# Optimization experiments

Measured on AMD Instinct MI355X. Metric: run time of the kernel, lower is better.

The kernel has to match this reference:

```python
import jax, jax.numpy as jnp
import numpy as np

LATENT, COND, NEURONS, NHID = 64, 96, 128, 3
EPS = 1e-5


def setup_inputs() -> dict:
    key = jax.random.key(0)
    ks = jax.random.split(key, 20)
    B, N = 1024, 512
    z0 = jax.random.normal(ks[0], (B, LATENT), jnp.float32)
    # monotone time grid in [0,1]
    t = jnp.cumsum(jax.random.uniform(ks[1], (B, N, 1), jnp.float32), axis=1)
    t = t / t[:, -1:, :]
    condition = jax.random.normal(ks[2], (B, N, COND), jnp.float32)
    dims = [LATENT + COND] + [NEURONS] * NHID
    inp = {"z0": z0, "t": t, "condition": condition}
    for i in range(NHID):
        din, dout = dims[i], dims[i + 1]
        inp[f"W{i}"] = jax.random.normal(ks[3 + 4 * i], (din, dout), jnp.float32) / np.sqrt(din)
        inp[f"b{i}"] = jnp.zeros((dout,), jnp.float32)
        inp[f"g{i}"] = jnp.ones((dout,), jnp.float32)
        inp[f"beta{i}"] = jnp.zeros((dout,), jnp.float32)
    inp["Wo"] = jax.random.normal(ks[16], (NEURONS, LATENT), jnp.float32) / np.sqrt(NEURONS)
    inp["bo"] = jnp.zeros((LATENT,), jnp.float32)
    return inp


def _layer_norm(x, g, b):
    mu = jnp.mean(x, axis=-1, keepdims=True)
    var = jnp.var(x, axis=-1, keepdims=True)
    return (x - mu) * jax.lax.rsqrt(var + EPS) * g + b


def reference(z0, t, condition,
              W0, b0, g0, beta0,
              W1, b1, g1, beta1,
              W2, b2, g2, beta2,
              Wo, bo):
    # dropout is inference-mode identity
    hidden = [(W0, b0, g0, beta0), (W1, b1, g1, beta1), (W2, b2, g2, beta2)]

    def mlp(x):
        h = x
        for (W, b, g, be) in hidden:
            h = jnp.tanh(_layer_norm(h @ W + b, g, be))
        return h @ Wo + bo

    # time-major sequences for scan: [N-1, B, ...]
    cond_seq = jnp.swapaxes(condition[:, :-1, :], 0, 1)
    dt_seq = jnp.swapaxes(t[:, 1:, 0] - t[:, :-1, 0], 0, 1)[..., None]

    def step(z, inp):
        cond_i, dt_i = inp
        dz = mlp(jnp.concatenate([z, cond_i], axis=-1))
        z_next = z + dt_i * dz
        return z_next, z_next

    _, zs = jax.lax.scan(step, z0, (cond_seq, dt_seq))  # [N-1, B, D]
    z_traj = jnp.concatenate([z0[None], zs], axis=0)  # [N, B, D]
    return jnp.swapaxes(z_traj, 0, 1)  # [B, N, D]
```

## Files before the change

### kernel.cpp

```cpp
#include <hip/hip_runtime.h>
#include <stdint.h>

#define NSEQ 512
#define XS 168
#define AS 136
#define PS 36
#define EPS 1e-5f

typedef short bfrag __attribute__((ext_vector_type(8)));
typedef float f4 __attribute__((ext_vector_type(4)));
#define MFMA16 __builtin_amdgcn_mfma_f32_16x16x32_bf16

__device__ __forceinline__ unsigned short f2bf(float f){
  uint32_t u = __float_as_uint(f);
  u += 0x7FFFu + ((u>>16)&1u);
  return (unsigned short)(u>>16);
}
__device__ __forceinline__ uint32_t pk2bf(float a, float b){
  uint32_t r;
  asm("v_cvt_pk_bf16_f32 %0, %1, %2" : "=v"(r) : "v"(a), "v"(b));
  return r;
}
__device__ __forceinline__ float tanh_fast(float v){
  float e = __builtin_amdgcn_exp2f(v * 2.8853900817779268f);
  float r = __builtin_amdgcn_rcpf(e + 1.f);
  return fmaf(-2.f, r, 1.f);
}
__device__ __forceinline__ void lds_barrier(){
  asm volatile("s_waitcnt lgkmcnt(0)" ::: "memory");
  __builtin_amdgcn_s_barrier();
  asm volatile("" ::: "memory");
}

__device__ __forceinline__ void stats_write(const float (&h0)[4], const float (&h1)[4],
                                            float* __restrict__ part,
                                            const int w, const int lg, const int lc){
  const float s = ((h0[0]+h0[1])+(h0[2]+h0[3])) + ((h1[0]+h1[1])+(h1[2]+h1[3]));
  const float q = (fmaf(h0[0],h0[0], h0[1]*h0[1]) + fmaf(h0[2],h0[2], h0[3]*h0[3]))
                + (fmaf(h1[0],h1[0], h1[1]*h1[1]) + fmaf(h1[2],h1[2], h1[3]*h1[3]));
  *(float2*)(part + lc*PS + (w*4+lg)*2) = make_float2(s, q);
}

__device__ __forceinline__ void ln_tanh_store(const float (&h0)[4], const float (&h1)[4],
    const float (&gd)[2][4], const float (&bed)[2][4],
    const float* __restrict__ part, unsigned short* __restrict__ actb,
    const int w, const int lg, const int lc){
  const float* pr = part + lc*PS;
  const f4 p0=*(const f4*)(pr),    p1=*(const f4*)(pr+4),  p2=*(const f4*)(pr+8),  p3=*(const f4*)(pr+12);
  const f4 p4=*(const f4*)(pr+16), p5=*(const f4*)(pr+20), p6=*(const f4*)(pr+24), p7=*(const f4*)(pr+28);
  const float ss = (((p0.x+p0.z)+(p1.x+p1.z)) + ((p2.x+p2.z)+(p3.x+p3.z)))
                 + (((p4.x+p4.z)+(p5.x+p5.z)) + ((p6.x+p6.z)+(p7.x+p7.z)));
  const float qq = (((p0.y+p0.w)+(p1.y+p1.w)) + ((p2.y+p2.w)+(p3.y+p3.w)))
                 + (((p4.y+p4.w)+(p5.y+p5.w)) + ((p6.y+p6.w)+(p7.y+p7.w)));
  const float mu = ss * 0.0078125f;
  const float rs = rsqrtf(fmaf(qq, 0.0078125f, -mu*mu) + EPS);
  float e0[4], e1[4];
#pragma unroll
  for (int g=0; g<4; ++g){
    e0[g] = tanh_fast(fmaf((h0[g]-mu)*rs, gd[0][g], bed[0][g]));
    e1[g] = tanh_fast(fmaf((h1[g]-mu)*rs, gd[1][g], bed[1][g]));
  }
  uint4 pk4;
  pk4.x = pk2bf(e0[0],e0[1]); pk4.y = pk2bf(e0[2],e0[3]);
  pk4.z = pk2bf(e1[0],e1[1]); pk4.w = pk2bf(e1[2],e1[3]);
  *(uint4*)(actb + lc*AS + w*32 + lg*8) = pk4;
}

__global__ __launch_bounds__(256, 1)
void latent_ode_v9(const float* __restrict__ z0, const float* __restrict__ tt,
                   const float* __restrict__ cond,
                   const float* __restrict__ W0, const float* __restrict__ b0,
                   const float* __restrict__ g0, const float* __restrict__ be0,
                   const float* __restrict__ W1, const float* __restrict__ b1,
                   const float* __restrict__ g1, const float* __restrict__ be1,
                   const float* __restrict__ W2, const float* __restrict__ b2,
                   const float* __restrict__ g2, const float* __restrict__ be2,
                   const float* __restrict__ Wo, const float* __restrict__ bo,
                   float* __restrict__ out)
{
  __shared__ __align__(16) unsigned short xin[16*XS];
  __shared__ __align__(16) unsigned short act[16*AS];
  __shared__ __align__(16) float part[16*PS];

  const int t  = threadIdx.x;
  const int w  = t >> 6;
  const int l  = t & 63;
  const int lg = l >> 4;
  const int lc = l & 15;
  const int r0 = blockIdx.x * 16;
  const int zcol = w*16 + lg*4;

  bfrag A0z[2][2], A0c[2][3], A1f[2][4], A2f[2][4], Aof[4];
#pragma unroll
  for (int nt=0; nt<2; ++nt){
    const int col = w*32 + nt*4 + ((lc>>2)<<3) + (lc&3);
#pragma unroll
    for (int kt=0; kt<2; ++kt){
      union { bfrag v; unsigned short u[8]; } r;
#pragma unroll
      for (int j=0; j<8; ++j) r.u[j] = f2bf(W0[(size_t)(kt*32 + lg*8 + j)*128 + col]);
      A0z[nt][kt] = r.v;
    }
#pragma unroll
    for (int s=0; s<3; ++s){
      union { bfrag v; unsigned short u[8]; } r;
#pragma unroll
      for (int j=0; j<8; ++j) r.u[j] = f2bf(W0[(size_t)(64 + s*32 + lg*8 + j)*128 + col]);
      A0c[nt][s] = r.v;
    }
#pragma unroll
    for (int kt=0; kt<4; ++kt){
      union { bfrag v; unsigned short u[8]; } r1, r2;
#pragma unroll
      for (int j=0; j<8; ++j){
        const int k = kt*32 + lg*8 + j;
        r1.u[j] = f2bf(W1[(size_t)k*128 + col]);
        r2.u[j] = f2bf(W2[(size_t)k*128 + col]);
      }
      A1f[nt][kt] = r1.v; A2f[nt][kt] = r2.v;
    }
  }
#pragma unroll
  for (int kt=0; kt<4; ++kt){
    union { bfrag v; unsigned short u[8]; } r;
#pragma unroll
    for (int j=0; j<8; ++j)
      r.u[j] = f2bf(Wo[(size_t)(kt*32 + lg*8 + j)*64 + (w*16 + lc)]);
    Aof[kt] = r.v;
  }
  float bd0[2][4], gd0[2][4], bed0[2][4];
  float bd1[2][4], gd1[2][4], bed1[2][4];
  float bd2[2][4], gd2[2][4], bed2[2][4];
  float bo_d[4];
#pragma unroll
  for (int nt=0; nt<2; ++nt){
#pragma unroll
    for (int g=0; g<4; ++g){
      const int n = w*32 + lg*8 + nt*4 + g;
      bd0[nt][g]=b0[n]; gd0[nt][g]=g0[n]; bed0[nt][g]=be0[n];
      bd1[nt][g]=b1[n]; gd1[nt][g]=g1[n]; bed1[nt][g]=be1[n];
      bd2[nt][g]=b2[n]; gd2[nt][g]=g2[n]; bed2[nt][g]=be2[n];
    }
  }
#pragma unroll
  for (int g=0; g<4; ++g) bo_d[g] = bo[zcol + g];

  const float* tp = tt + (size_t)(r0+lc)*NSEQ;
  float tcv = tp[0], tnv = tp[1];

  f4 zr;
  {
    const f4 zv = *(const f4*)(z0 + (size_t)(r0+lc)*64 + zcol);
    zr = zv;
    *(f4*)(out + ((size_t)(r0+lc)*NSEQ)*64 + zcol) = zv;
    *(uint2*)(xin + lc*XS + zcol) = make_uint2(pk2bf(zv[0],zv[1]), pk2bf(zv[2],zv[3]));
  }

  const bool stgW = (t < 192);
  const int srow = t / 12, s8 = t - srow*12;
  const float* cptr = cond + ((size_t)(r0+srow)*NSEQ)*96 + s8*8;
  float4 pf0 = {0,0,0,0}, pf1 = {0,0,0,0};
  if (stgW){
    const float4 c0 = *(const float4*)(cptr);
    const float4 c1 = *(const float4*)(cptr + 4);
    uint4 u;
    u.x = pk2bf(c0.x,c0.y); u.y = pk2bf(c0.z,c0.w);
    u.z = pk2bf(c1.x,c1.y); u.w = pk2bf(c1.z,c1.w);
    *(uint4*)(xin + srow*XS + 64 + s8*8) = u;
    pf0 = *(const float4*)(cptr + 96);
    pf1 = *(const float4*)(cptr + 100);
  }
  lds_barrier();

  f4 apC[2];
  {
    const int o = lc*XS + 64 + lg*8;
    const bfrag c0 = *(const bfrag*)(xin + o);
    const bfrag c1 = *(const bfrag*)(xin + o + 32);
    const bfrag c2 = *(const bfrag*)(xin + o + 64);
    const f4 z4 = {0,0,0,0};
#pragma unroll
    for (int nt=0; nt<2; ++nt){
      f4 a = MFMA16(A0c[nt][0], c0, z4, 0,0,0);
      a = MFMA16(A0c[nt][1], c1, a, 0,0,0);
      a = MFMA16(A0c[nt][2], c2, a, 0,0,0);
      apC[nt] = a;
    }
  }
  lds_barrier();

  float h0[4], h1[4];
  for (int i=0; i<NSEQ-1; ++i){
    const int ip2 = (i+2 <= NSEQ-1) ? (i+2) : (NSEQ-1);
    const float tfv = tp[ip2];
    {
      const int o = lc*XS + lg*8;
      const bfrag bz0 = *(const bfrag*)(xin + o);
      const bfrag bz1 = *(const bfrag*)(xin + o + 32);
      const f4 z4 = {0,0,0,0};
      f4 c0 = MFMA16(A0z[0][0], bz0, z4, 0,0,0);
      f4 c1 = MFMA16(A0z[1][0], bz0, z4, 0,0,0);
      c0 = MFMA16(A0z[0][1], bz1, c0, 0,0,0);
      c1 = MFMA16(A0z[1][1], bz1, c1, 0,0,0);
#pragma unroll
      for (int g=0; g<4; ++g){
        h0[g] = (c0[g] + apC[0][g]) + bd0[0][g];
        h1[g] = (c1[g] + apC[1][g]) + bd0[1][g];
      }
      stats_write(h0, h1, part, w, lg, lc);
    }
    if (stgW){
      uint4 u;
      u.x = pk2bf(pf0.x,pf0.y); u.y = pk2bf(pf0.z,pf0.w);
      u.z = pk2bf(pf1.x,pf1.y); u.w = pk2bf(pf1.z,pf1.w);
      *(uint4*)(xin + srow*XS + 64 + s8*8) = u;
      if (i < NSEQ-2){
        pf0 = *(const float4*)(cptr + (size_t)(i+2)*96);
        pf1 = *(const float4*)(cptr + (size_t)(i+2)*96 + 4);
      }
    }
    lds_barrier();

    {
      const int o = lc*XS + 64 + lg*8;
      const bfrag c0 = *(const bfrag*)(xin + o);
      const bfrag c1 = *(const bfrag*)(xin + o + 32);
      const bfrag c2 = *(const bfrag*)(xin + o + 64);
      const f4 z4 = {0,0,0,0};
      f4 a0 = MFMA16(A0c[0][0], c0, z4, 0,0,0);
      f4 a1 = MFMA16(A0c[1][0], c0, z4, 0,0,0);
      a0 = MFMA16(A0c[0][1], c1, a0, 0,0,0);
      a1 = MFMA16(A0c[1][1], c1, a1, 0,0,0);
      a0 = MFMA16(A0c[0][2], c2, a0, 0,0,0);
      a1 = MFMA16(A0c[1][2], c2, a1, 0,0,0);
      ln_tanh_store(h0, h1, gd0, bed0, part, act, w, lg, lc);
      apC[0] = a0; apC[1] = a1;
    }
    lds_barrier();

    {
      const int o = lc*AS + lg*8;
      const bfrag b0f = *(const bfrag*)(act + o);
      const bfrag b1f = *(const bfrag*)(act + o + 32);
      const bfrag b2f = *(const bfrag*)(act + o + 64);
      const bfrag b3f = *(const bfrag*)(act + o + 96);
      const f4 z4 = {0,0,0,0};
      f4 ca0 = MFMA16(A1f[0][0], b0f, z4, 0,0,0);
      f4 cb0 = MFMA16(A1f[0][1], b1f, z4, 0,0,0);
      f4 ca1 = MFMA16(A1f[1][0], b0f, z4, 0,0,0);
      f4 cb1 = MFMA16(A1f[1][1], b1f, z4, 0,0,0);
      ca0 = MFMA16(A1f[0][2], b2f, ca0, 0,0,0);
      cb0 = MFMA16(A1f[0][3], b3f, cb0, 0,0,0);
      ca1 = MFMA16(A1f[1][2], b2f, ca1, 0,0,0);
      cb1 = MFMA16(A1f[1][3], b3f, cb1, 0,0,0);
#pragma unroll
      for (int g=0; g<4; ++g){
        h0[g] = (ca0[g]+cb0[g]) + bd1[0][g];
        h1[g] = (ca1[g]+cb1[g]) + bd1[1][g];
      }
      stats_write(h0, h1, part, w, lg, lc);
    }
    lds_barrier();

    ln_tanh_store(h0, h1, gd1, bed1, part, act, w, lg, lc);
    lds_barrier();

    {
      const int o = lc*AS + lg*8;
      const bfrag b0f = *(const bfrag*)(act + o);
      const bfrag b1f = *(const bfrag*)(act + o + 32);
      const bfrag b2f = *(const bfrag*)(act + o + 64);
      const bfrag b3f = *(const bfrag*)(act + o + 96);
      const f4 z4 = {0,0,0,0};
      f4 ca0 = MFMA16(A2f[0][0], b0f, z4, 0,0,0);
      f4 cb0 = MFMA16(A2f[0][1], b1f, z4, 0,0,0);
      f4 ca1 = MFMA16(A2f[1][0], b0f, z4, 0,0,0);
      f4 cb1 = MFMA16(A2f[1][1], b1f, z4, 0,0,0);
      ca0 = MFMA16(A2f[0][2], b2f, ca0, 0,0,0);
      cb0 = MFMA16(A2f[0][3], b3f, cb0, 0,0,0);
      ca1 = MFMA16(A2f[1][2], b2f, ca1, 0,0,0);
      cb1 = MFMA16(A2f[1][3], b3f, cb1, 0,0,0);
#pragma unroll
      for (int g=0; g<4; ++g){
        h0[g] = (ca0[g]+cb0[g]) + bd2[0][g];
        h1[g] = (ca1[g]+cb1[g]) + bd2[1][g];
      }
      stats_write(h0, h1, part, w, lg, lc);
    }
    lds_barrier();

    ln_tanh_store(h0, h1, gd2, bed2, part, act, w, lg, lc);
    lds_barrier();

    {
      const int o = lc*AS + lg*8;
      const bfrag b0f = *(const bfrag*)(act + o);
      const bfrag b1f = *(const bfrag*)(act + o + 32);
      const bfrag b2f = *(const bfrag*)(act + o + 64);
      const bfrag b3f = *(const bfrag*)(act + o + 96);
      const f4 z4 = {0,0,0,0};
      f4 aa = MFMA16(Aof[0], b0f, z4, 0,0,0);
      f4 ab = MFMA16(Aof[1], b1f, z4, 0,0,0);
      aa = MFMA16(Aof[2], b2f, aa, 0,0,0);
      ab = MFMA16(Aof[3], b3f, ab, 0,0,0);
      const float dt = tnv - tcv;
      f4 zn;
#pragma unroll
      for (int g=0; g<4; ++g) zn[g] = fmaf(dt, (aa[g]+ab[g]) + bo_d[g], zr[g]);
      zr = zn;
      *(f4*)(out + ((size_t)(r0+lc)*NSEQ + (size_t)(i+1))*64 + zcol) = zn;
      *(uint2*)(xin + lc*XS + zcol) = make_uint2(pk2bf(zn[0],zn[1]), pk2bf(zn[2],zn[3]));
      tcv = tnv; tnv = tfv;
    }
    lds_barrier();
  }
}

extern "C" void kernel_launch(void* const* d_in, const int* in_sizes, int n_in,
                              void* d_out, int out_size, void* d_ws, size_t ws_size,
                              hipStream_t stream) {
  const float* z0   = (const float*)d_in[0];
  const float* tt   = (const float*)d_in[1];
  const float* cond = (const float*)d_in[2];
  const float* W0   = (const float*)d_in[3];
  const float* b0   = (const float*)d_in[4];
  const float* g0   = (const float*)d_in[5];
  const float* be0  = (const float*)d_in[6];
  const float* W1   = (const float*)d_in[7];
  const float* b1   = (const float*)d_in[8];
  const float* g1   = (const float*)d_in[9];
  const float* be1  = (const float*)d_in[10];
  const float* W2   = (const float*)d_in[11];
  const float* b2   = (const float*)d_in[12];
  const float* g2   = (const float*)d_in[13];
  const float* be2  = (const float*)d_in[14];
  const float* Wo   = (const float*)d_in[15];
  const float* bo   = (const float*)d_in[16];
  float* out = (float*)d_out;

  hipLaunchKernelGGL(latent_ode_v9, dim3(64), dim3(256), 0, stream,
                     z0, tt, cond, W0, b0, g0, be0, W1, b1, g1, be1,
                     W2, b2, g2, be2, Wo, bo, out);
}
```

Baseline: 1.111 ms.

## Compute output layer redundantly per wave to keep z in registers and drop a barrier

Each wave now computes the full 64-column output projection (four times the MFMAs), so every wave holds the whole updated z in registers in the fragment layout that the next step's layer-0 MFMA needs. The z half of layer 0 and its LN stats are then computed at the end of the same phase, which removes the z round-trip through LDS and one barrier per timestep. The condition staging is moved into the same phase and the xin row stride shrinks. The cost is redundant output-layer MFMAs and more registers held for the Wo fragments.

```diff
diff --git a/kernel.cpp b/kernel.cpp
--- a/kernel.cpp
+++ b/kernel.cpp
@@ -2,7 +2,7 @@
 #include <stdint.h>
 
 #define NSEQ 512
-#define XS 168
+#define XS 104
 #define AS 136
 #define PS 36
 #define EPS 1e-5f
@@ -67,16 +67,16 @@
 }
 
 __global__ __launch_bounds__(256, 1)
-void latent_ode_v9(const float* __restrict__ z0, const float* __restrict__ tt,
-                   const float* __restrict__ cond,
-                   const float* __restrict__ W0, const float* __restrict__ b0,
-                   const float* __restrict__ g0, const float* __restrict__ be0,
-                   const float* __restrict__ W1, const float* __restrict__ b1,
-                   const float* __restrict__ g1, const float* __restrict__ be1,
-                   const float* __restrict__ W2, const float* __restrict__ b2,
-                   const float* __restrict__ g2, const float* __restrict__ be2,
-                   const float* __restrict__ Wo, const float* __restrict__ bo,
-                   float* __restrict__ out)
+void latent_ode_v10(const float* __restrict__ z0, const float* __restrict__ tt,
+                    const float* __restrict__ cond,
+                    const float* __restrict__ W0, const float* __restrict__ b0,
+                    const float* __restrict__ g0, const float* __restrict__ be0,
+                    const float* __restrict__ W1, const float* __restrict__ b1,
+                    const float* __restrict__ g1, const float* __restrict__ be1,
+                    const float* __restrict__ W2, const float* __restrict__ b2,
+                    const float* __restrict__ g2, const float* __restrict__ be2,
+                    const float* __restrict__ Wo, const float* __restrict__ bo,
+                    float* __restrict__ out)
 {
   __shared__ __align__(16) unsigned short xin[16*XS];
   __shared__ __align__(16) unsigned short act[16*AS];
@@ -88,9 +88,8 @@
   const int lg = l >> 4;
   const int lc = l & 15;
   const int r0 = blockIdx.x * 16;
-  const int zcol = w*16 + lg*4;
-
-  bfrag A0z[2][2], A0c[2][3], A1f[2][4], A2f[2][4], Aof[4];
+
+  bfrag A0z[2][2], A0c[2][3], A1f[2][4], A2f[2][4];
 #pragma unroll
   for (int nt=0; nt<2; ++nt){
     const int col = w*32 + nt*4 + ((lc>>2)<<3) + (lc&3);
@@ -120,18 +119,23 @@
       A1f[nt][kt] = r1.v; A2f[nt][kt] = r2.v;
     }
   }
-#pragma unroll
-  for (int kt=0; kt<4; ++kt){
-    union { bfrag v; unsigned short u[8]; } r;
-#pragma unroll
-    for (int j=0; j<8; ++j)
-      r.u[j] = f2bf(Wo[(size_t)(kt*32 + lg*8 + j)*64 + (w*16 + lc)]);
-    Aof[kt] = r.v;
+  bfrag Aof[4][4];
+#pragma unroll
+  for (int nt=0; nt<4; ++nt){
+    const int colM = (nt&1)*32 + ((lc>>2)<<3) + ((nt>>1)<<2) + (lc&3);
+#pragma unroll
+    for (int kt=0; kt<4; ++kt){
+      union { bfrag v; unsigned short u[8]; } r;
+#pragma unroll
+      for (int j=0; j<8; ++j)
+        r.u[j] = f2bf(Wo[(size_t)(kt*32 + lg*8 + j)*64 + colM]);
+      Aof[nt][kt] = r.v;
+    }
   }
   float bd0[2][4], gd0[2][4], bed0[2][4];
   float bd1[2][4], gd1[2][4], bed1[2][4];
   float bd2[2][4], gd2[2][4], bed2[2][4];
-  float bo_d[4];
+  float bo_d[4][4];
 #pragma unroll
   for (int nt=0; nt<2; ++nt){
 #pragma unroll
@@ -143,17 +147,28 @@
     }
   }
 #pragma unroll
-  for (int g=0; g<4; ++g) bo_d[g] = bo[zcol + g];
+  for (int nt=0; nt<4; ++nt)
+#pragma unroll
+    for (int g=0; g<4; ++g)
+      bo_d[nt][g] = bo[(nt&1)*32 + lg*8 + ((nt>>1)<<2) + g];
 
   const float* tp = tt + (size_t)(r0+lc)*NSEQ;
   float tcv = tp[0], tnv = tp[1];
 
-  f4 zr;
+  f4 zr[4];
+  union { bfrag v; uint32_t u[4]; } zu0, zu1;
   {
-    const f4 zv = *(const f4*)(z0 + (size_t)(r0+lc)*64 + zcol);
-    zr = zv;
-    *(f4*)(out + ((size_t)(r0+lc)*NSEQ)*64 + zcol) = zv;
-    *(uint2*)(xin + lc*XS + zcol) = make_uint2(pk2bf(zv[0],zv[1]), pk2bf(zv[2],zv[3]));
+    float* ob0 = out + ((size_t)(r0+lc)*NSEQ)*64;
+#pragma unroll
+    for (int nt=0; nt<4; ++nt){
+      const int lb = (nt&1)*32 + lg*8 + ((nt>>1)<<2);
+      zr[nt] = *(const f4*)(z0 + (size_t)(r0+lc)*64 + lb);
+      *(f4*)(ob0 + lb) = zr[nt];
+    }
+    zu0.u[0]=pk2bf(zr[0][0],zr[0][1]); zu0.u[1]=pk2bf(zr[0][2],zr[0][3]);
+    zu0.u[2]=pk2bf(zr[2][0],zr[2][1]); zu0.u[3]=pk2bf(zr[2][2],zr[2][3]);
+    zu1.u[0]=pk2bf(zr[1][0],zr[1][1]); zu1.u[1]=pk2bf(zr[1][2],zr[1][3]);
+    zu1.u[2]=pk2bf(zr[3][0],zr[3][1]); zu1.u[3]=pk2bf(zr[3][2],zr[3][3]);
   }
 
   const bool stgW = (t < 192);
@@ -166,15 +181,16 @@
     uint4 u;
     u.x = pk2bf(c0.x,c0.y); u.y = pk2bf(c0.z,c0.w);
     u.z = pk2bf(c1.x,c1.y); u.w = pk2bf(c1.z,c1.w);
-    *(uint4*)(xin + srow*XS + 64 + s8*8) = u;
+    *(uint4*)(xin + srow*XS + s8*8) = u;
     pf0 = *(const float4*)(cptr + 96);
     pf1 = *(const float4*)(cptr + 100);
   }
   lds_barrier();
 
   f4 apC[2];
+  float h0[4], h1[4];
   {
-    const int o = lc*XS + 64 + lg*8;
+    const int o = lc*XS + lg*8;
     const bfrag c0 = *(const bfrag*)(xin + o);
     const bfrag c1 = *(const bfrag*)(xin + o + 32);
     const bfrag c2 = *(const bfrag*)(xin + o + 64);
@@ -186,43 +202,31 @@
       a = MFMA16(A0c[nt][2], c2, a, 0,0,0);
       apC[nt] = a;
     }
+    f4 d0 = MFMA16(A0z[0][0], zu0.v, z4, 0,0,0);
+    f4 d1 = MFMA16(A0z[1][0], zu0.v, z4, 0,0,0);
+    d0 = MFMA16(A0z[0][1], zu1.v, d0, 0,0,0);
+    d1 = MFMA16(A0z[1][1], zu1.v, d1, 0,0,0);
+#pragma unroll
+    for (int g=0; g<4; ++g){
+      h0[g] = (d0[g] + apC[0][g]) + bd0[0][g];
+      h1[g] = (d1[g] + apC[1][g]) + bd0[1][g];
+    }
+    stats_write(h0, h1, part, w, lg, lc);
   }
   lds_barrier();
-
-  float h0[4], h1[4];
+  if (stgW){
+    uint4 u;
+    u.x = pk2bf(pf0.x,pf0.y); u.y = pk2bf(pf0.z,pf0.w);
+    u.z = pk2bf(pf1.x,pf1.y); u.w = pk2bf(pf1.z,pf1.w);
+    *(uint4*)(xin + srow*XS + s8*8) = u;
+    pf0 = *(const float4*)(cptr + 2*96);
+    pf1 = *(const float4*)(cptr + 2*96 + 4);
+  }
+  lds_barrier();
+
   for (int i=0; i<NSEQ-1; ++i){
-    const int ip2 = (i+2 <= NSEQ-1) ? (i+2) : (NSEQ-1);
-    const float tfv = tp[ip2];
     {
       const int o = lc*XS + lg*8;
-      const bfrag bz0 = *(const bfrag*)(xin + o);
-      const bfrag bz1 = *(const bfrag*)(xin + o + 32);
-      const f4 z4 = {0,0,0,0};
-      f4 c0 = MFMA16(A0z[0][0], bz0, z4, 0,0,0);
-      f4 c1 = MFMA16(A0z[1][0], bz0, z4, 0,0,0);
-      c0 = MFMA16(A0z[0][1], bz1, c0, 0,0,0);
-      c1 = MFMA16(A0z[1][1], bz1, c1, 0,0,0);
-#pragma unroll
-      for (int g=0; g<4; ++g){
-        h0[g] = (c0[g] + apC[0][g]) + bd0[0][g];
-        h1[g] = (c1[g] + apC[1][g]) + bd0[1][g];
-      }
-      stats_write(h0, h1, part, w, lg, lc);
-    }
-    if (stgW){
-      uint4 u;
-      u.x = pk2bf(pf0.x,pf0.y); u.y = pk2bf(pf0.z,pf0.w);
-      u.z = pk2bf(pf1.x,pf1.y); u.w = pk2bf(pf1.z,pf1.w);
-      *(uint4*)(xin + srow*XS + 64 + s8*8) = u;
-      if (i < NSEQ-2){
-        pf0 = *(const float4*)(cptr + (size_t)(i+2)*96);
-        pf1 = *(const float4*)(cptr + (size_t)(i+2)*96 + 4);
-      }
-    }
-    lds_barrier();
-
-    {
-      const int o = lc*XS + 64 + lg*8;
       const bfrag c0 = *(const bfrag*)(xin + o);
       const bfrag c1 = *(const bfrag*)(xin + o + 32);
       const bfrag c2 = *(const bfrag*)(xin + o + 64);
@@ -293,23 +297,57 @@
     lds_barrier();
 
     {
+      const int ip2 = (i+2 <= NSEQ-1) ? (i+2) : (NSEQ-1);
+      const float tfv = tp[ip2];
       const int o = lc*AS + lg*8;
       const bfrag b0f = *(const bfrag*)(act + o);
       const bfrag b1f = *(const bfrag*)(act + o + 32);
       const bfrag b2f = *(const bfrag*)(act + o + 64);
       const bfrag b3f = *(const bfrag*)(act + o + 96);
       const f4 z4 = {0,0,0,0};
-      f4 aa = MFMA16(Aof[0], b0f, z4, 0,0,0);
-      f4 ab = MFMA16(Aof[1], b1f, z4, 0,0,0);
-      aa = MFMA16(Aof[2], b2f, aa, 0,0,0);
-      ab = MFMA16(Aof[3], b3f, ab, 0,0,0);
       const float dt = tnv - tcv;
-      f4 zn;
-#pragma unroll
-      for (int g=0; g<4; ++g) zn[g] = fmaf(dt, (aa[g]+ab[g]) + bo_d[g], zr[g]);
-      zr = zn;
-      *(f4*)(out + ((size_t)(r0+lc)*NSEQ + (size_t)(i+1))*64 + zcol) = zn;
-      *(uint2*)(xin + lc*XS + zcol) = make_uint2(pk2bf(zn[0],zn[1]), pk2bf(zn[2],zn[3]));
+      f4 zn[4];
+#pragma unroll
+      for (int nt=0; nt<4; ++nt){
+        f4 aa = MFMA16(Aof[nt][0], b0f, z4, 0,0,0);
+        f4 ab = MFMA16(Aof[nt][1], b1f, z4, 0,0,0);
+        aa = MFMA16(Aof[nt][2], b2f, aa, 0,0,0);
+        ab = MFMA16(Aof[nt][3], b3f, ab, 0,0,0);
+#pragma unroll
+        for (int g=0; g<4; ++g)
+          zn[nt][g] = fmaf(dt, (aa[g]+ab[g]) + bo_d[nt][g], zr[nt][g]);
+        zr[nt] = zn[nt];
+      }
+      float* ob = out + ((size_t)(r0+lc)*NSEQ + (size_t)(i+1))*64;
+#pragma unroll
+      for (int nt=0; nt<4; ++nt)
+        *(f4*)(ob + (nt&1)*32 + lg*8 + ((nt>>1)<<2)) = zn[nt];
+      zu0.u[0]=pk2bf(zn[0][0],zn[0][1]); zu0.u[1]=pk2bf(zn[0][2],zn[0][3]);
+      zu0.u[2]=pk2bf(zn[2][0],zn[2][1]); zu0.u[3]=pk2bf(zn[2][2],zn[2][3]);
+      zu1.u[0]=pk2bf(zn[1][0],zn[1][1]); zu1.u[1]=pk2bf(zn[1][2],zn[1][3]);
+      zu1.u[2]=pk2bf(zn[3][0],zn[3][1]); zu1.u[3]=pk2bf(zn[3][2],zn[3][3]);
+      if (i < NSEQ-2){
+        f4 d0 = MFMA16(A0z[0][0], zu0.v, z4, 0,0,0);
+        f4 d1 = MFMA16(A0z[1][0], zu0.v, z4, 0,0,0);
+        d0 = MFMA16(A0z[0][1], zu1.v, d0, 0,0,0);
+        d1 = MFMA16(A0z[1][1], zu1.v, d1, 0,0,0);
+#pragma unroll
+        for (int g=0; g<4; ++g){
+          h0[g] = (d0[g] + apC[0][g]) + bd0[0][g];
+          h1[g] = (d1[g] + apC[1][g]) + bd0[1][g];
+        }
+        stats_write(h0, h1, part, w, lg, lc);
+        if (stgW){
+          uint4 u;
+          u.x = pk2bf(pf0.x,pf0.y); u.y = pk2bf(pf0.z,pf0.w);
+          u.z = pk2bf(pf1.x,pf1.y); u.w = pk2bf(pf1.z,pf1.w);
+          *(uint4*)(xin + srow*XS + s8*8) = u;
+          if (i < NSEQ-3){
+            pf0 = *(const float4*)(cptr + (size_t)(i+3)*96);
+            pf1 = *(const float4*)(cptr + (size_t)(i+3)*96 + 4);
+          }
+        }
+      }
       tcv = tnv; tnv = tfv;
     }
     lds_barrier();
@@ -338,7 +376,7 @@
   const float* bo   = (const float*)d_in[16];
   float* out = (float*)d_out;
 
-  hipLaunchKernelGGL(latent_ode_v9, dim3(64), dim3(256), 0, stream,
+  hipLaunchKernelGGL(latent_ode_v10, dim3(64), dim3(256), 0, stream,
                      z0, tt, cond, W0, b0, g0, be0, W1, b1, g1, be1,
                      W2, b2, g2, be2, Wo, bo, out);
 }
```

New measurement: 1.717 ms. 54.5% more time.

## Split output projection by K across waves and keep z replicated in registers

Applied to the files above, without the earlier changes.

The last layer's LayerNorm+tanh result now stays in registers as the B fragment. Each wave computes a partial product over its own 32-wide K slice of Wo for all 64 outputs and writes it to a new LDS buffer. Every wave then reduces the four partials and applies the Euler update on its own replicated copy of z, which removes one barrier and the act-buffer round trip per step, and feeds z to the first layer straight from registers instead of LDS. In exchange it adds redundant reduction work in every wave, extra LDS traffic for the partials, and a peeled final step.

```diff
diff --git a/kernel.cpp b/kernel.cpp
--- a/kernel.cpp
+++ b/kernel.cpp
@@ -2,9 +2,10 @@
 #include <stdint.h>
 
 #define NSEQ 512
-#define XS 168
+#define XS 104
 #define AS 136
 #define PS 36
+#define LS 68
 #define EPS 1e-5f
 
 typedef short bfrag __attribute__((ext_vector_type(8)));
@@ -41,10 +42,8 @@
   *(float2*)(part + lc*PS + (w*4+lg)*2) = make_float2(s, q);
 }
 
-__device__ __forceinline__ void ln_tanh_store(const float (&h0)[4], const float (&h1)[4],
-    const float (&gd)[2][4], const float (&bed)[2][4],
-    const float* __restrict__ part, unsigned short* __restrict__ actb,
-    const int w, const int lg, const int lc){
+__device__ __forceinline__ void ln_mu_rs(const float* __restrict__ part, const int lc,
+                                         float& mu, float& rs){
   const float* pr = part + lc*PS;
   const f4 p0=*(const f4*)(pr),    p1=*(const f4*)(pr+4),  p2=*(const f4*)(pr+8),  p3=*(const f4*)(pr+12);
   const f4 p4=*(const f4*)(pr+16), p5=*(const f4*)(pr+20), p6=*(const f4*)(pr+24), p7=*(const f4*)(pr+28);
@@ -52,8 +51,16 @@
                  + (((p4.x+p4.z)+(p5.x+p5.z)) + ((p6.x+p6.z)+(p7.x+p7.z)));
   const float qq = (((p0.y+p0.w)+(p1.y+p1.w)) + ((p2.y+p2.w)+(p3.y+p3.w)))
                  + (((p4.y+p4.w)+(p5.y+p5.w)) + ((p6.y+p6.w)+(p7.y+p7.w)));
-  const float mu = ss * 0.0078125f;
-  const float rs = rsqrtf(fmaf(qq, 0.0078125f, -mu*mu) + EPS);
+  mu = ss * 0.0078125f;
+  rs = rsqrtf(fmaf(qq, 0.0078125f, -mu*mu) + EPS);
+}
+
+__device__ __forceinline__ void ln_tanh_store(const float (&h0)[4], const float (&h1)[4],
+    const float (&gd)[2][4], const float (&bed)[2][4],
+    const float* __restrict__ part, unsigned short* __restrict__ actb,
+    const int w, const int lg, const int lc){
+  float mu, rs;
+  ln_mu_rs(part, lc, mu, rs);
   float e0[4], e1[4];
 #pragma unroll
   for (int g=0; g<4; ++g){
@@ -66,21 +73,39 @@
   *(uint4*)(actb + lc*AS + w*32 + lg*8) = pk4;
 }
 
+__device__ __forceinline__ bfrag ln_tanh_own(const float (&h0)[4], const float (&h1)[4],
+    const float (&gd)[2][4], const float (&bed)[2][4],
+    const float* __restrict__ part, const int lc){
+  float mu, rs;
+  ln_mu_rs(part, lc, mu, rs);
+  float e0[4], e1[4];
+#pragma unroll
+  for (int g=0; g<4; ++g){
+    e0[g] = tanh_fast(fmaf((h0[g]-mu)*rs, gd[0][g], bed[0][g]));
+    e1[g] = tanh_fast(fmaf((h1[g]-mu)*rs, gd[1][g], bed[1][g]));
+  }
+  union { bfrag v; uint32_t u[4]; } r;
+  r.u[0]=pk2bf(e0[0],e0[1]); r.u[1]=pk2bf(e0[2],e0[3]);
+  r.u[2]=pk2bf(e1[0],e1[1]); r.u[3]=pk2bf(e1[2],e1[3]);
+  return r.v;
+}
+
 __global__ __launch_bounds__(256, 1)
-void latent_ode_v9(const float* __restrict__ z0, const float* __restrict__ tt,
-                   const float* __restrict__ cond,
-                   const float* __restrict__ W0, const float* __restrict__ b0,
-                   const float* __restrict__ g0, const float* __restrict__ be0,
-                   const float* __restrict__ W1, const float* __restrict__ b1,
-                   const float* __restrict__ g1, const float* __restrict__ be1,
-                   const float* __restrict__ W2, const float* __restrict__ b2,
-                   const float* __restrict__ g2, const float* __restrict__ be2,
-                   const float* __restrict__ Wo, const float* __restrict__ bo,
-                   float* __restrict__ out)
+void latent_ode_v13(const float* __restrict__ z0, const float* __restrict__ tt,
+                    const float* __restrict__ cond,
+                    const float* __restrict__ W0, const float* __restrict__ b0,
+                    const float* __restrict__ g0, const float* __restrict__ be0,
+                    const float* __restrict__ W1, const float* __restrict__ b1,
+                    const float* __restrict__ g1, const float* __restrict__ be1,
+                    const float* __restrict__ W2, const float* __restrict__ b2,
+                    const float* __restrict__ g2, const float* __restrict__ be2,
+                    const float* __restrict__ Wo, const float* __restrict__ bo,
+                    float* __restrict__ out)
 {
   __shared__ __align__(16) unsigned short xin[16*XS];
   __shared__ __align__(16) unsigned short act[16*AS];
   __shared__ __align__(16) float part[16*PS];
+  __shared__ __align__(16) float lop[4*16*LS];
 
   const int t  = threadIdx.x;
   const int w  = t >> 6;
@@ -88,9 +113,8 @@
   const int lg = l >> 4;
   const int lc = l & 15;
   const int r0 = blockIdx.x * 16;
-  const int zcol = w*16 + lg*4;
-
-  bfrag A0z[2][2], A0c[2][3], A1f[2][4], A2f[2][4], Aof[4];
+
+  bfrag A0z[2][2], A0c[2][3], A1f[2][4], A2f[2][4];
 #pragma unroll
   for (int nt=0; nt<2; ++nt){
     const int col = w*32 + nt*4 + ((lc>>2)<<3) + (lc&3);
@@ -120,18 +144,18 @@
       A1f[nt][kt] = r1.v; A2f[nt][kt] = r2.v;
     }
   }
-#pragma unroll
-  for (int kt=0; kt<4; ++kt){
+  bfrag Aof[4];
+#pragma unroll
+  for (int nt=0; nt<4; ++nt){
     union { bfrag v; unsigned short u[8]; } r;
 #pragma unroll
     for (int j=0; j<8; ++j)
-      r.u[j] = f2bf(Wo[(size_t)(kt*32 + lg*8 + j)*64 + (w*16 + lc)]);
-    Aof[kt] = r.v;
+      r.u[j] = f2bf(Wo[(size_t)(w*32 + lg*8 + j)*64 + (nt*16 + lc)]);
+    Aof[nt] = r.v;
   }
   float bd0[2][4], gd0[2][4], bed0[2][4];
   float bd1[2][4], gd1[2][4], bed1[2][4];
   float bd2[2][4], gd2[2][4], bed2[2][4];
-  float bo_d[4];
 #pragma unroll
   for (int nt=0; nt<2; ++nt){
 #pragma unroll
@@ -142,18 +166,33 @@
       bd2[nt][g]=b2[n]; gd2[nt][g]=g2[n]; bed2[nt][g]=be2[n];
     }
   }
-#pragma unroll
-  for (int g=0; g<4; ++g) bo_d[g] = bo[zcol + g];
+  f4 bo0a = *(const f4*)(bo + 8*lg);
+  f4 bo0b = *(const f4*)(bo + 8*lg + 4);
+  f4 bo1a = *(const f4*)(bo + 32 + 8*lg);
+  f4 bo1b = *(const f4*)(bo + 32 + 8*lg + 4);
 
   const float* tp = tt + (size_t)(r0+lc)*NSEQ;
-  float tcv = tp[0], tnv = tp[1];
-
-  f4 zr;
+  float tcv = 0.f, tnv = tp[0];
+
+  f4 za0, za1, zb0, zb1;
+  bfrag Bz0, Bz1;
   {
-    const f4 zv = *(const f4*)(z0 + (size_t)(r0+lc)*64 + zcol);
-    zr = zv;
-    *(f4*)(out + ((size_t)(r0+lc)*NSEQ)*64 + zcol) = zv;
-    *(uint2*)(xin + lc*XS + zcol) = make_uint2(pk2bf(zv[0],zv[1]), pk2bf(zv[2],zv[3]));
+    const float* zp = z0 + (size_t)(r0+lc)*64;
+    za0 = *(const f4*)(zp + 8*lg);
+    za1 = *(const f4*)(zp + 8*lg + 4);
+    zb0 = *(const f4*)(zp + 32 + 8*lg);
+    zb1 = *(const f4*)(zp + 32 + 8*lg + 4);
+    if (w == 0){
+      float* op = out + ((size_t)(r0+lc)*NSEQ)*64;
+      *(f4*)(op + 8*lg) = za0;  *(f4*)(op + 8*lg + 4) = za1;
+      *(f4*)(op + 32 + 8*lg) = zb0;  *(f4*)(op + 32 + 8*lg + 4) = zb1;
+    }
+    union { bfrag v; uint32_t u[4]; } a, b;
+    a.u[0]=pk2bf(za0[0],za0[1]); a.u[1]=pk2bf(za0[2],za0[3]);
+    a.u[2]=pk2bf(za1[0],za1[1]); a.u[3]=pk2bf(za1[2],za1[3]);
+    b.u[0]=pk2bf(zb0[0],zb0[1]); b.u[1]=pk2bf(zb0[2],zb0[3]);
+    b.u[2]=pk2bf(zb1[0],zb1[1]); b.u[3]=pk2bf(zb1[2],zb1[3]);
+    Bz0=a.v; Bz1=b.v;
   }
 
   const bool stgW = (t < 192);
@@ -166,7 +205,7 @@
     uint4 u;
     u.x = pk2bf(c0.x,c0.y); u.y = pk2bf(c0.z,c0.w);
     u.z = pk2bf(c1.x,c1.y); u.w = pk2bf(c1.z,c1.w);
-    *(uint4*)(xin + srow*XS + 64 + s8*8) = u;
+    *(uint4*)(xin + srow*XS + s8*8) = u;
     pf0 = *(const float4*)(cptr + 96);
     pf1 = *(const float4*)(cptr + 100);
   }
@@ -174,7 +213,7 @@
 
   f4 apC[2];
   {
-    const int o = lc*XS + 64 + lg*8;
+    const int o = lc*XS + lg*8;
     const bfrag c0 = *(const bfrag*)(xin + o);
     const bfrag c1 = *(const bfrag*)(xin + o + 32);
     const bfrag c2 = *(const bfrag*)(xin + o + 64);
@@ -191,17 +230,63 @@
 
   float h0[4], h1[4];
   for (int i=0; i<NSEQ-1; ++i){
-    const int ip2 = (i+2 <= NSEQ-1) ? (i+2) : (NSEQ-1);
-    const float tfv = tp[ip2];
+    const float tfv = tp[i+1];
+    if (i > 0){
+      const float dt = tnv - tcv;
+      {
+        const float* lpA = lop + lc*LS + 8*lg;
+        const f4 p0 = *(const f4*)(lpA);
+        const f4 p1 = *(const f4*)(lpA + 16*LS);
+        const f4 p2 = *(const f4*)(lpA + 32*LS);
+        const f4 p3 = *(const f4*)(lpA + 48*LS);
+        const f4 q0 = *(const f4*)(lpA + 4);
+        const f4 q1 = *(const f4*)(lpA + 16*LS + 4);
+        const f4 q2 = *(const f4*)(lpA + 32*LS + 4);
+        const f4 q3 = *(const f4*)(lpA + 48*LS + 4);
+        const f4 dza = (((p0+p1)+p2)+p3) + bo0a;
+        const f4 dzb = (((q0+q1)+q2)+q3) + bo0b;
+#pragma unroll
+        for (int g=0; g<4; ++g){
+          za0[g] = fmaf(dt, dza[g], za0[g]);
+          za1[g] = fmaf(dt, dzb[g], za1[g]);
+        }
+      }
+      {
+        const float* lpB = lop + lc*LS + 32 + 8*lg;
+        const f4 p0 = *(const f4*)(lpB);
+        const f4 p1 = *(const f4*)(lpB + 16*LS);
+        const f4 p2 = *(const f4*)(lpB + 32*LS);
+        const f4 p3 = *(const f4*)(lpB + 48*LS);
+        const f4 q0 = *(const f4*)(lpB + 4);
+        const f4 q1 = *(const f4*)(lpB + 16*LS + 4);
+        const f4 q2 = *(const f4*)(lpB + 32*LS + 4);
+        const f4 q3 = *(const f4*)(lpB + 48*LS + 4);
+        const f4 dza = (((p0+p1)+p2)+p3) + bo1a;
+        const f4 dzb = (((q0+q1)+q2)+q3) + bo1b;
+#pragma unroll
+        for (int g=0; g<4; ++g){
+          zb0[g] = fmaf(dt, dza[g], zb0[g]);
+          zb1[g] = fmaf(dt, dzb[g], zb1[g]);
+        }
+      }
+      if (w == 0){
+        float* op = out + ((size_t)(r0+lc)*NSEQ + (size_t)i)*64;
+        *(f4*)(op + 8*lg) = za0;  *(f4*)(op + 8*lg + 4) = za1;
+        *(f4*)(op + 32 + 8*lg) = zb0;  *(f4*)(op + 32 + 8*lg + 4) = zb1;
+      }
+      union { bfrag v; uint32_t u[4]; } a, b;
+      a.u[0]=pk2bf(za0[0],za0[1]); a.u[1]=pk2bf(za0[2],za0[3]);
+      a.u[2]=pk2bf(za1[0],za1[1]); a.u[3]=pk2bf(za1[2],za1[3]);
+      b.u[0]=pk2bf(zb0[0],zb0[1]); b.u[1]=pk2bf(zb0[2],zb0[3]);
+      b.u[2]=pk2bf(zb1[0],zb1[1]); b.u[3]=pk2bf(zb1[2],zb1[3]);
+      Bz0=a.v; Bz1=b.v;
+    }
     {
-      const int o = lc*XS + lg*8;
-      const bfrag bz0 = *(const bfrag*)(xin + o);
-      const bfrag bz1 = *(const bfrag*)(xin + o + 32);
       const f4 z4 = {0,0,0,0};
-      f4 c0 = MFMA16(A0z[0][0], bz0, z4, 0,0,0);
-      f4 c1 = MFMA16(A0z[1][0], bz0, z4, 0,0,0);
-      c0 = MFMA16(A0z[0][1], bz1, c0, 0,0,0);
-      c1 = MFMA16(A0z[1][1], bz1, c1, 0,0,0);
+      f4 c0 = MFMA16(A0z[0][0], Bz0, z4, 0,0,0);
+      f4 c1 = MFMA16(A0z[1][0], Bz0, z4, 0,0,0);
+      c0 = MFMA16(A0z[0][1], Bz1, c0, 0,0,0);
+      c1 = MFMA16(A0z[1][1], Bz1, c1, 0,0,0);
 #pragma unroll
       for (int g=0; g<4; ++g){
         h0[g] = (c0[g] + apC[0][g]) + bd0[0][g];
@@ -213,16 +298,17 @@
       uint4 u;
       u.x = pk2bf(pf0.x,pf0.y); u.y = pk2bf(pf0.z,pf0.w);
       u.z = pk2bf(pf1.x,pf1.y); u.w = pk2bf(pf1.z,pf1.w);
-      *(uint4*)(xin + srow*XS + 64 + s8*8) = u;
+      *(uint4*)(xin + srow*XS + s8*8) = u;
       if (i < NSEQ-2){
         pf0 = *(const float4*)(cptr + (size_t)(i+2)*96);
         pf1 = *(const float4*)(cptr + (size_t)(i+2)*96 + 4);
       }
     }
+    tcv = tnv; tnv = tfv;
     lds_barrier();
 
     {
-      const int o = lc*XS + 64 + lg*8;
+      const int o = lc*XS + lg*8;
       const bfrag c0 = *(const bfrag*)(xin + o);
       const bfrag c1 = *(const bfrag*)(xin + o + 32);
       const bfrag c2 = *(const bfrag*)(xin + o + 64);
@@ -289,30 +375,58 @@
     }
     lds_barrier();
 
-    ln_tanh_store(h0, h1, gd2, bed2, part, act, w, lg, lc);
-    lds_barrier();
-
     {
-      const int o = lc*AS + lg*8;
-      const bfrag b0f = *(const bfrag*)(act + o);
-      const bfrag b1f = *(const bfrag*)(act + o + 32);
-      const bfrag b2f = *(const bfrag*)(act + o + 64);
-      const bfrag b3f = *(const bfrag*)(act + o + 96);
+      const bfrag Bown = ln_tanh_own(h0, h1, gd2, bed2, part, lc);
       const f4 z4 = {0,0,0,0};
-      f4 aa = MFMA16(Aof[0], b0f, z4, 0,0,0);
-      f4 ab = MFMA16(Aof[1], b1f, z4, 0,0,0);
-      aa = MFMA16(Aof[2], b2f, aa, 0,0,0);
-      ab = MFMA16(Aof[3], b3f, ab, 0,0,0);
-      const float dt = tnv - tcv;
-      f4 zn;
-#pragma unroll
-      for (int g=0; g<4; ++g) zn[g] = fmaf(dt, (aa[g]+ab[g]) + bo_d[g], zr[g]);
-      zr = zn;
-      *(f4*)(out + ((size_t)(r0+lc)*NSEQ + (size_t)(i+1))*64 + zcol) = zn;
-      *(uint2*)(xin + lc*XS + zcol) = make_uint2(pk2bf(zn[0],zn[1]), pk2bf(zn[2],zn[3]));
-      tcv = tnv; tnv = tfv;
-    }
-    lds_barrier();
+      f4 lp0 = MFMA16(Aof[0], Bown, z4, 0,0,0);
+      f4 lp1 = MFMA16(Aof[1], Bown, z4, 0,0,0);
+      f4 lp2 = MFMA16(Aof[2], Bown, z4, 0,0,0);
+      f4 lp3 = MFMA16(Aof[3], Bown, z4, 0,0,0);
+      float* lw = lop + (size_t)w*16*LS + lc*LS + lg*4;
+      *(f4*)(lw)      = lp0;
+      *(f4*)(lw + 16) = lp1;
+      *(f4*)(lw + 32) = lp2;
+      *(f4*)(lw + 48) = lp3;
+    }
+    lds_barrier();
+  }
+
+  {
+    const float dt = tnv - tcv;
+    if (w == 0){
+      const float* lpA = lop + lc*LS + 8*lg;
+      const f4 p0 = *(const f4*)(lpA);
+      const f4 p1 = *(const f4*)(lpA + 16*LS);
+      const f4 p2 = *(const f4*)(lpA + 32*LS);
+      const f4 p3 = *(const f4*)(lpA + 48*LS);
+      const f4 q0 = *(const f4*)(lpA + 4);
+      const f4 q1 = *(const f4*)(lpA + 16*LS + 4);
+      const f4 q2 = *(const f4*)(lpA + 32*LS + 4);
+      const f4 q3 = *(const f4*)(lpA + 48*LS + 4);
+      const f4 dza = (((p0+p1)+p2)+p3) + bo0a;
+      const f4 dzb = (((q0+q1)+q2)+q3) + bo0b;
+      const float* lpB = lop + lc*LS + 32 + 8*lg;
+      const f4 r0v = *(const f4*)(lpB);
+      const f4 r1v = *(const f4*)(lpB + 16*LS);
+      const f4 r2v = *(const f4*)(lpB + 32*LS);
+      const f4 r3v = *(const f4*)(lpB + 48*LS);
+      const f4 s0v = *(const f4*)(lpB + 4);
+      const f4 s1v = *(const f4*)(lpB + 16*LS + 4);
+      const f4 s2v = *(const f4*)(lpB + 32*LS + 4);
+      const f4 s3v = *(const f4*)(lpB + 48*LS + 4);
+      const f4 dzc = (((r0v+r1v)+r2v)+r3v) + bo1a;
+      const f4 dzd = (((s0v+s1v)+s2v)+s3v) + bo1b;
+#pragma unroll
+      for (int g=0; g<4; ++g){
+        za0[g] = fmaf(dt, dza[g], za0[g]);
+        za1[g] = fmaf(dt, dzb[g], za1[g]);
+        zb0[g] = fmaf(dt, dzc[g], zb0[g]);
+        zb1[g] = fmaf(dt, dzd[g], zb1[g]);
+      }
+      float* op = out + ((size_t)(r0+lc)*NSEQ + (size_t)(NSEQ-1))*64;
+      *(f4*)(op + 8*lg) = za0;  *(f4*)(op + 8*lg + 4) = za1;
+      *(f4*)(op + 32 + 8*lg) = zb0;  *(f4*)(op + 32 + 8*lg + 4) = zb1;
+    }
   }
 }
 
@@ -338,7 +452,7 @@
   const float* bo   = (const float*)d_in[16];
   float* out = (float*)d_out;
 
-  hipLaunchKernelGGL(latent_ode_v9, dim3(64), dim3(256), 0, stream,
+  hipLaunchKernelGGL(latent_ode_v13, dim3(64), dim3(256), 0, stream,
                      z0, tt, cond, W0, b0, g0, be0, W1, b1, g1, be1,
                      W2, b2, g2, be2, Wo, bo, out);
 }
```

New measurement: 1.272 ms. +14.4%, slower.
